# Kernel optimization log

Measured on AMD Instinct MI355X. Metric: run time of the kernel, lower is better.

The kernel has to match this reference:

```python
import jax, jax.numpy as jnp
import numpy as np

B, S, H, I, L, NH = 1, 256, 384, 1536, 2, 8

def _gelu(x):
    return jax.nn.gelu(x, approximate=False)  # torch nn.GELU default = exact erf

def _ln(x, g, b, eps=1e-5):
    m = x.mean(-1, keepdims=True)
    v = jnp.var(x, axis=-1, keepdims=True)
    return (x - m) / jnp.sqrt(v + eps) * g + b

def _mha(x, Wqkv, bqkv, Wo, bo):
    b_, s_, h_ = x.shape
    d = h_ // NH
    qkv = x @ Wqkv.T + bqkv  # [B,S,3H]
    q, k, v = jnp.split(qkv, 3, axis=-1)
    sp = lambda t: t.reshape(b_, s_, NH, d).transpose(0, 2, 1, 3)  # [B,NH,S,d]
    q, k, v = sp(q), sp(k), sp(v)
    att = jax.nn.softmax(jnp.einsum('bhqd,bhkd->bhqk', q * (1.0 / np.sqrt(d)), k), axis=-1)
    o = jnp.einsum('bhqk,bhkd->bhqd', att, v).transpose(0, 2, 1, 3).reshape(b_, s_, h_)
    return o @ Wo.T + bo

def _forward(hidden_states, Wqkv, bqkv, Wo, bo, W1, b1, W2, b2, g1, be1, g2, be2,
             Wbil, bbil, Wc1, bc1, Wc2, bc2, Wih, bih, Whh, bhh, Wp1, bp1, Wp2, bp2,
             Wout, bout, reasoning_steps):
    x = hidden_states
    rstate = jnp.zeros((x.shape[0], x.shape[-1]), x.dtype)
    cprobs, conts = [], []
    for _ in range(reasoning_steps):
        # symbolic reasoning layers (eval mode: dropout off)
        for l in range(L):
            x = _ln(x + _mha(x, Wqkv[l], bqkv[l], Wo[l], bo[l]), g1[l], be1[l])
            ff = _gelu(x @ W1[l].T + b1[l]) @ W2[l].T + b2[l]
            x = _ln(x + ff, g2[l], be2[l])
        # contradiction detector: bilinear over all token pairs
        tmp = jnp.einsum('bix,oxy->bioy', x, Wbil)            # [B,S,H,H]
        inter = jnp.einsum('bioy,bjy->bijo', tmp, x) + bbil   # [B,S,S,H]
        h1 = _gelu(inter @ Wc1.T + bc1)                       # [B,S,S,H]
        logits = jnp.einsum('bijh,h->bij', h1, Wc2[0]) + bc2[0]
        cprobs.append(jax.nn.sigmoid(logits))
        # recursive reasoning controller (GRUCell on mean-pooled states)
        pooled = x.mean(axis=1)
        gi = pooled @ Wih.T + bih
        gh = rstate @ Whh.T + bhh
        ir, iz, inn = jnp.split(gi, 3, axis=-1)
        hr, hz, hn = jnp.split(gh, 3, axis=-1)
        r = jax.nn.sigmoid(ir + hr)
        z = jax.nn.sigmoid(iz + hz)
        n = jnp.tanh(inn + r * hn)
        rstate = (1.0 - z) * n + z * rstate
        conts.append(jax.nn.sigmoid(_gelu(rstate @ Wp1.T + bp1) @ Wp2[0] + bp2[0]))
    final = x @ Wout.T + bout
    return final, jnp.stack(cprobs), jnp.stack(conts)

def setup_inputs():
    key = jax.random.key(0)
    ks = iter(jax.random.split(key, 40))
    rn = lambda shape, s=0.02: jax.random.normal(next(ks), shape, jnp.float32) * s
    return {
        'hidden_states': jax.random.normal(next(ks), (B, S, H), jnp.float32),
        'Wqkv': rn((L, 3 * H, H)), 'bqkv': jnp.zeros((L, 3 * H)),
        'Wo': rn((L, H, H)), 'bo': jnp.zeros((L, H)),
        'W1': rn((L, I, H)), 'b1': jnp.zeros((L, I)),
        'W2': rn((L, H, I)), 'b2': jnp.zeros((L, H)),
        'g1': jnp.ones((L, H)), 'be1': jnp.zeros((L, H)),
        'g2': jnp.ones((L, H)), 'be2': jnp.zeros((L, H)),
        'Wbil': rn((H, H, H)), 'bbil': jnp.zeros((H,)),
        'Wc1': rn((H, H)), 'bc1': jnp.zeros((H,)),
        'Wc2': rn((1, H)), 'bc2': jnp.zeros((1,)),
        'Wih': rn((3 * H, H)), 'bih': jnp.zeros((3 * H,)),
        'Whh': rn((3 * H, H)), 'bhh': jnp.zeros((3 * H,)),
        'Wp1': rn((H, H)), 'bp1': jnp.zeros((H,)),
        'Wp2': rn((1, H)), 'bp2': jnp.zeros((1,)),
        'Wout': rn((H, H)), 'bout': jnp.zeros((H,)),
        'reasoning_steps': 2,
    }

def reference(hidden_states, Wqkv, bqkv, Wo, bo, W1, b1, W2, b2, g1, be1, g2, be2,
              Wbil, bbil, Wc1, bc1, Wc2, bc2, Wih, bih, Whh, bhh, Wp1, bp1, Wp2, bp2,
              Wout, bout, reasoning_steps):
    return _forward(hidden_states, Wqkv, bqkv, Wo, bo, W1, b1, W2, b2, g1, be1, g2, be2,
                    Wbil, bbil, Wc1, bc1, Wc2, bc2, Wih, bih, Whh, bhh, Wp1, bp1, Wp2, bp2,
                    Wout, bout, reasoning_steps)
```

## Files before the change

kernel.cpp:

```cpp
#include <hip/hip_runtime.h>

typedef __attribute__((ext_vector_type(4))) float f32x4;
typedef __attribute__((ext_vector_type(8))) short s16x8;

#define DEVI __device__ __forceinline__

DEVI float b2f(short s) {
  union { float f; unsigned u; } v; v.u = ((unsigned)(unsigned short)s) << 16; return v.f;
}
DEVI short f2b(float f) {
  union { float f; unsigned u; } v; v.f = f;
  unsigned u = v.u;
  u += 0x7FFFu + ((u >> 16) & 1u);
  return (short)(u >> 16);
}
DEVI float gelu_f(float x) {
  float z2 = 1.5957691216f * x * (1.0f + 0.044715f * x * x);
  float e = __expf(z2);
  float th = 1.0f - 2.0f / (e + 1.0f);
  return 0.5f * x * (1.0f + th);
}
DEVI float sigm_f(float x) { return 1.0f / (1.0f + expf(-x)); }

DEVI void gld16(const short* g, const short* l) {
  __builtin_amdgcn_global_load_lds((const __attribute__((address_space(1))) void*)g,
                                   (__attribute__((address_space(3))) void*)l, 16, 0, 0);
}

template<bool BIAS, bool GELU_ACT, bool OUT_BF16>
__global__ __launch_bounds__(256)
void gemm_fast_k(const short* __restrict__ A, const short* __restrict__ B,
                 const float* __restrict__ bias, void* __restrict__ Cv,
                 int M, int N, int K,
                 long long sA, long long sB, long long sC)
{
  __shared__ short As[2][128 * 32];
  __shared__ short Bs[2][128 * 32];
  const int bz = blockIdx.z;
  const int n0 = blockIdx.x * 128;
  const int m0 = blockIdx.y * 128;
  const int t = threadIdx.x, lane = t & 63, wave = t >> 6;
  const int wm = wave >> 1, wn = wave & 1;
  const short* Ab = A + bz * sA;
  const short* Bb = B + bz * sB;
  const int srow = lane >> 2;
  const int scol = (lane & 3) * 8;
  const int fr = lane & 15, fs = lane >> 4;

  f32x4 acc[4][4];
#pragma unroll
  for (int i = 0; i < 4; ++i)
#pragma unroll
    for (int j = 0; j < 4; ++j) acc[i][j] = f32x4{0.f, 0.f, 0.f, 0.f};

  auto stage = [&](int b, int k0) {
#pragma unroll
    for (int q = 0; q < 2; ++q) {
      int c = wave * 2 + q;
      gld16(Ab + (long long)(m0 + c * 16 + srow) * K + k0 + scol, &As[b][c * 512]);
      gld16(Bb + (long long)(n0 + c * 16 + srow) * K + k0 + scol, &Bs[b][c * 512]);
    }
  };

  const int NT = K >> 5;
  stage(0, 0);
  __syncthreads();
  for (int tt = 0; tt < NT; ++tt) {
    const int cur = tt & 1;
    if (tt + 1 < NT) stage(cur ^ 1, (tt + 1) << 5);
    s16x8 af[4], bfv[4];
#pragma unroll
    for (int i = 0; i < 4; ++i) af[i]  = *(const s16x8*)&As[cur][(wm * 64 + i * 16 + fr) * 32 + fs * 8];
#pragma unroll
    for (int j = 0; j < 4; ++j) bfv[j] = *(const s16x8*)&Bs[cur][(wn * 64 + j * 16 + fr) * 32 + fs * 8];
#pragma unroll
    for (int i = 0; i < 4; ++i)
#pragma unroll
      for (int j = 0; j < 4; ++j)
        acc[i][j] = __builtin_amdgcn_mfma_f32_16x16x32_bf16(af[i], bfv[j], acc[i][j], 0, 0, 0);
    if (tt + 1 < NT) __syncthreads();
  }

#pragma unroll
  for (int i = 0; i < 4; ++i) {
    int rowb = m0 + wm * 64 + i * 16 + fs * 4;
#pragma unroll
    for (int j = 0; j < 4; ++j) {
      int col = n0 + wn * 64 + j * 16 + fr;
      float bb = BIAS ? bias[col] : 0.0f;
#pragma unroll
      for (int u = 0; u < 4; ++u) {
        float v = acc[i][j][u] + bb;
        if constexpr (GELU_ACT) v = gelu_f(v);
        long long off = bz * sC + (long long)(rowb + u) * N + col;
        if constexpr (OUT_BF16) ((short*)Cv)[off] = f2b(v);
        else                    ((float*)Cv)[off] = v;
      }
    }
  }
}

template<bool BIAS, bool GELU_ACT, bool OUT_BF16>
__global__ __launch_bounds__(256)
void gemm64_k(const short* __restrict__ A, const short* __restrict__ B,
              const float* __restrict__ bias, void* __restrict__ Cv,
              int M, int N, int K)
{
  __shared__ short As[2][64 * 32];
  __shared__ short Bs[2][64 * 32];
  const int n0 = blockIdx.x * 64;
  const int m0 = blockIdx.y * 64;
  const int t = threadIdx.x, lane = t & 63, wave = t >> 6;
  const int wm = wave >> 1, wn = wave & 1;
  const int srow = lane >> 2;
  const int scol = (lane & 3) * 8;
  const int fr = lane & 15, fs = lane >> 4;

  f32x4 acc[2][2];
#pragma unroll
  for (int i = 0; i < 2; ++i)
#pragma unroll
    for (int j = 0; j < 2; ++j) acc[i][j] = f32x4{0.f, 0.f, 0.f, 0.f};

  auto stage = [&](int b, int k0) {
    gld16(A + (long long)(m0 + wave * 16 + srow) * K + k0 + scol, &As[b][wave * 512]);
    gld16(B + (long long)(n0 + wave * 16 + srow) * K + k0 + scol, &Bs[b][wave * 512]);
  };

  const int NT = K >> 5;
  stage(0, 0);
  __syncthreads();
  for (int tt = 0; tt < NT; ++tt) {
    const int cur = tt & 1;
    if (tt + 1 < NT) stage(cur ^ 1, (tt + 1) << 5);
    s16x8 af[2], bfv[2];
#pragma unroll
    for (int i = 0; i < 2; ++i) af[i]  = *(const s16x8*)&As[cur][(wm * 32 + i * 16 + fr) * 32 + fs * 8];
#pragma unroll
    for (int j = 0; j < 2; ++j) bfv[j] = *(const s16x8*)&Bs[cur][(wn * 32 + j * 16 + fr) * 32 + fs * 8];
#pragma unroll
    for (int i = 0; i < 2; ++i)
#pragma unroll
      for (int j = 0; j < 2; ++j)
        acc[i][j] = __builtin_amdgcn_mfma_f32_16x16x32_bf16(af[i], bfv[j], acc[i][j], 0, 0, 0);
    if (tt + 1 < NT) __syncthreads();
  }

#pragma unroll
  for (int i = 0; i < 2; ++i) {
    int rowb = m0 + wm * 32 + i * 16 + fs * 4;
#pragma unroll
    for (int j = 0; j < 2; ++j) {
      int col = n0 + wn * 32 + j * 16 + fr;
      float bb = BIAS ? bias[col] : 0.0f;
#pragma unroll
      for (int u = 0; u < 4; ++u) {
        float v = acc[i][j][u] + bb;
        if constexpr (GELU_ACT) v = gelu_f(v);
        long long off = (long long)(rowb + u) * N + col;
        if constexpr (OUT_BF16) ((short*)Cv)[off] = f2b(v);
        else                    ((float*)Cv)[off] = v;
      }
    }
  }
}

__global__ __launch_bounds__(256)
void transpose_k(const float* __restrict__ W, short* __restrict__ WT)
{
  __shared__ short L[64 * 68];
  const int o  = blockIdx.z;
  const int x0 = blockIdx.x * 64, y0 = blockIdx.y * 64;
  const float* Wo = W  + (long long)o * 147456;
  short*      WTo = WT + (long long)o * 147456;
  const int t  = threadIdx.x;
  const int rr = t >> 4;
  const int cc = (t & 15) * 4;
#pragma unroll
  for (int q = 0; q < 4; ++q) {
    int xl = rr + 16 * q;
    float4 v = *(const float4*)(Wo + (x0 + xl) * 384 + y0 + cc);
    short4 p; p.x = f2b(v.x); p.y = f2b(v.y); p.z = f2b(v.z); p.w = f2b(v.w);
    *(short4*)&L[xl * 68 + cc] = p;
  }
  __syncthreads();
#pragma unroll
  for (int q = 0; q < 4; ++q) {
    int yl = rr + 16 * q;
    short4 p;
    p.x = L[(cc + 0) * 68 + yl];
    p.y = L[(cc + 1) * 68 + yl];
    p.z = L[(cc + 2) * 68 + yl];
    p.w = L[(cc + 3) * 68 + yl];
    *(short4*)(WTo + (y0 + yl) * 384 + x0 + cc) = p;
  }
}

__global__ __launch_bounds__(256)
void convw_k(const float* __restrict__ W, short* __restrict__ Wb, int n)
{
  int i = (blockIdx.x * 256 + threadIdx.x) * 4;
  if (i < n) {
    float4 v = *(const float4*)(W + i);
    short4 p; p.x = f2b(v.x); p.y = f2b(v.y); p.z = f2b(v.z); p.w = f2b(v.w);
    *(short4*)(Wb + i) = p;
  }
}

__global__ __launch_bounds__(256)
void attn_k(const float* __restrict__ qkv, short* __restrict__ outb)
{
  __shared__ short Ks[256 * 48];
  __shared__ short Vs[256 * 48];
  __shared__ float Ps[32][258];
  const int h  = blockIdx.y;
  const int q0 = blockIdx.x * 32;
  const int t = threadIdx.x, lane = t & 63, wave = t >> 6;
  for (int idx = t; idx < 256 * 48; idx += 256) {
    int j = idx / 48, d = idx - j * 48;
    Ks[idx] = f2b(qkv[j * 1152 + 384 + h * 48 + d]);
    Vs[idx] = f2b(qkv[j * 1152 + 768 + h * 48 + d]);
  }
  __syncthreads();
  const int part = lane & 7;
  const int rl   = wave * 8 + (lane >> 3);
  const int row  = q0 + rl;
  float q[48];
#pragma unroll
  for (int d = 0; d < 48; ++d) q[d] = qkv[row * 1152 + h * 48 + d] * 0.14433756729740644f;
  float mx = -1e30f;
  for (int jj = 0; jj < 32; ++jj) {
    int j = jj * 8 + part;
    float a = 0.f;
#pragma unroll
    for (int dd = 0; dd < 12; ++dd) {
      short4 kk = *(const short4*)&Ks[j * 48 + dd * 4];
      a += q[dd*4+0]*b2f(kk.x) + q[dd*4+1]*b2f(kk.y) + q[dd*4+2]*b2f(kk.z) + q[dd*4+3]*b2f(kk.w);
    }
    Ps[rl][j] = a;
    mx = fmaxf(mx, a);
  }
  mx = fmaxf(mx, __shfl_xor(mx, 1));
  mx = fmaxf(mx, __shfl_xor(mx, 2));
  mx = fmaxf(mx, __shfl_xor(mx, 4));
  float sum = 0.f;
  for (int jj = 0; jj < 32; ++jj) {
    int j = jj * 8 + part;
    float e = expf(Ps[rl][j] - mx);
    Ps[rl][j] = e;
    sum += e;
  }
  sum += __shfl_xor(sum, 1); sum += __shfl_xor(sum, 2); sum += __shfl_xor(sum, 4);
  const float inv = 1.f / sum;
  __syncthreads();
  float o[6] = {0.f, 0.f, 0.f, 0.f, 0.f, 0.f};
  const int vb = part * 6;
  for (int j = 0; j < 256; ++j) {
    float p = Ps[rl][j];
    int base = j * 48 + vb;
#pragma unroll
    for (int dd = 0; dd < 3; ++dd) {
      short2 vv = *(const short2*)&Vs[base + dd * 2];
      o[dd*2]   += p * b2f(vv.x);
      o[dd*2+1] += p * b2f(vv.y);
    }
  }
#pragma unroll
  for (int d = 0; d < 6; ++d) outb[row * 384 + h * 48 + vb + d] = f2b(o[d] * inv);
}

__global__ __launch_bounds__(128)
void ln_k(const float* __restrict__ x, const float* __restrict__ d,
          const float* __restrict__ g, const float* __restrict__ b,
          float* __restrict__ xo, short* __restrict__ xob)
{
  const int row = blockIdx.x, t = threadIdx.x;
  float v[3]; float s = 0.f, ss = 0.f;
#pragma unroll
  for (int i = 0; i < 3; ++i) {
    int c = t + 128 * i;
    float u = x[row * 384 + c] + d[row * 384 + c];
    v[i] = u; s += u; ss += u * u;
  }
#pragma unroll
  for (int m = 1; m < 64; m <<= 1) { s += __shfl_xor(s, m); ss += __shfl_xor(ss, m); }
  __shared__ float sh[4];
  if ((t & 63) == 0) { sh[(t >> 6) * 2] = s; sh[(t >> 6) * 2 + 1] = ss; }
  __syncthreads();
  s = sh[0] + sh[2]; ss = sh[1] + sh[3];
  float mean = s * (1.f / 384.f);
  float var  = ss * (1.f / 384.f) - mean * mean;
  float rstd = rsqrtf(var + 1e-5f);
#pragma unroll
  for (int i = 0; i < 3; ++i) {
    int c = t + 128 * i;
    float y = (v[i] - mean) * rstd * g[c] + b[c];
    xo[row * 384 + c]  = y;
    xob[row * 384 + c] = f2b(y);
  }
}

__global__ void init_k(const float* __restrict__ hs, float* __restrict__ x,
                       short* __restrict__ xb, float* __restrict__ rstate)
{
  int i = blockIdx.x * 256 + threadIdx.x;
  if (i < 98304) { float v = hs[i]; x[i] = v; xb[i] = f2b(v); }
  if (i < 384) rstate[i] = 0.f;
}

__global__ __launch_bounds__(256)
void logits_k(const short* __restrict__ h1, const float* __restrict__ Wc2,
              const float* __restrict__ bc2, float* __restrict__ outp)
{
  const int t = threadIdx.x, lane = t & 63, wave = t >> 6;
  const int row = blockIdx.x * 4 + wave;
  const short* hr = h1 + (long long)row * 384;
  float a = 0.f;
#pragma unroll
  for (int e = 0; e < 6; ++e) { int c = lane + 64 * e; a += b2f(hr[c]) * Wc2[c]; }
#pragma unroll
  for (int m = 1; m < 64; m <<= 1) a += __shfl_xor(a, m);
  if (lane == 0) outp[row] = sigm_f(a + bc2[0]);
}

__global__ __launch_bounds__(384)
void pool1_k(const float* __restrict__ x, float* __restrict__ partial)
{
  const int t = threadIdx.x, p = blockIdx.x;
  float s = 0.f;
  const float* xr = x + p * 32 * 384;
#pragma unroll 4
  for (int i = 0; i < 32; ++i) s += xr[i * 384 + t];
  partial[p * 384 + t] = s;
}

__global__ __launch_bounds__(256)
void gih_k(const float* __restrict__ Wih, const float* __restrict__ bih,
           const float* __restrict__ Whh, const float* __restrict__ bhh,
           const float* __restrict__ partial, const float* __restrict__ rstate,
           float* __restrict__ gi, float* __restrict__ gh)
{
  const int t = threadIdx.x, lane = t & 63, wave = t >> 6;
  const int r = blockIdx.x * 4 + wave;
  float a = 0.f, b = 0.f;
#pragma unroll
  for (int e = 0; e < 6; ++e) {
    int c = lane + 64 * e;
    float pc = 0.f;
#pragma unroll
    for (int p = 0; p < 8; ++p) pc += partial[p * 384 + c];
    pc *= (1.f / 256.f);
    a += Wih[r * 384 + c] * pc;
    b += Whh[r * 384 + c] * rstate[c];
  }
#pragma unroll
  for (int m = 1; m < 64; m <<= 1) { a += __shfl_xor(a, m); b += __shfl_xor(b, m); }
  if (lane == 0) { gi[r] = a + bih[r]; gh[r] = b + bhh[r]; }
}

__global__ __launch_bounds__(384)
void gru2_k(const float* __restrict__ gi, const float* __restrict__ gh,
            float* __restrict__ rstate, float* __restrict__ hnew)
{
  const int t = threadIdx.x;
  float r = sigm_f(gi[t] + gh[t]);
  float z = sigm_f(gi[384 + t] + gh[384 + t]);
  float n = tanhf(gi[768 + t] + r * gh[768 + t]);
  float h = (1.f - z) * n + z * rstate[t];
  rstate[t] = h;
  hnew[t] = h;
}

__global__ __launch_bounds__(256)
void p1_k(const float* __restrict__ Wp1, const float* __restrict__ bp1,
          const float* __restrict__ hnew, float* __restrict__ p1)
{
  const int t = threadIdx.x, lane = t & 63, wave = t >> 6;
  const int r = blockIdx.x * 4 + wave;
  float a = 0.f;
#pragma unroll
  for (int e = 0; e < 6; ++e) { int c = lane + 64 * e; a += Wp1[r * 384 + c] * hnew[c]; }
#pragma unroll
  for (int m = 1; m < 64; m <<= 1) a += __shfl_xor(a, m);
  if (lane == 0) p1[r] = gelu_f(a + bp1[r]);
}

__global__ __launch_bounds__(64)
void cont_k(const float* __restrict__ p1, const float* __restrict__ Wp2,
            const float* __restrict__ bp2, float* __restrict__ out_cont)
{
  const int lane = threadIdx.x;
  float a = 0.f;
#pragma unroll
  for (int e = 0; e < 6; ++e) { int c = lane + 64 * e; a += p1[c] * Wp2[c]; }
#pragma unroll
  for (int m = 1; m < 64; m <<= 1) a += __shfl_xor(a, m);
  if (lane == 0) out_cont[0] = sigm_f(a + bp2[0]);
}

extern "C" void kernel_launch(void* const* d_in, const int* in_sizes, int n_in,
                              void* d_out, int out_size, void* d_ws, size_t ws_size,
                              hipStream_t stream)
{
  const float* hs   = (const float*)d_in[0];
  const float* Wqkv = (const float*)d_in[1];
  const float* bqkv = (const float*)d_in[2];
  const float* Wo   = (const float*)d_in[3];
  const float* bo   = (const float*)d_in[4];
  const float* W1   = (const float*)d_in[5];
  const float* b1   = (const float*)d_in[6];
  const float* W2   = (const float*)d_in[7];
  const float* b2   = (const float*)d_in[8];
  const float* g1   = (const float*)d_in[9];
  const float* be1  = (const float*)d_in[10];
  const float* g2   = (const float*)d_in[11];
  const float* be2  = (const float*)d_in[12];
  const float* Wbil = (const float*)d_in[13];
  const float* bbil = (const float*)d_in[14];
  const float* Wc1  = (const float*)d_in[15];
  const float* bc1  = (const float*)d_in[16];
  const float* Wc2  = (const float*)d_in[17];
  const float* bc2  = (const float*)d_in[18];
  const float* Wih  = (const float*)d_in[19];
  const float* bih  = (const float*)d_in[20];
  const float* Whh  = (const float*)d_in[21];
  const float* bhh  = (const float*)d_in[22];
  const float* Wp1  = (const float*)d_in[23];
  const float* bp1  = (const float*)d_in[24];
  const float* Wp2  = (const float*)d_in[25];
  const float* bp2  = (const float*)d_in[26];
  const float* Wout = (const float*)d_in[27];
  const float* bout = (const float*)d_in[28];
  float* out = (float*)d_out;

  char* ws = (char*)d_ws;
  size_t off = 0;
  auto alloc = [&](size_t bytes) -> char* {
    char* p = ws + off; off += (bytes + 255) & ~(size_t)255; return p;
  };
  short* wbilT   = (short*)alloc(56623104ULL * 2);
  short* tmp     = (short*)alloc(256ULL * 147456 * 2);
  short* inter   = (short*)alloc(256ULL * 98304 * 2);
  float* x       = (float*)alloc(98304 * 4);
  short* xb      = (short*)alloc(98304 * 2);
  float* qkv     = (float*)alloc(294912 * 4);
  short* attnb   = (short*)alloc(98304 * 2);
  float* delta   = (float*)alloc(98304 * 4);
  short* ff1b    = (short*)alloc(393216 * 2);
  float* rstate  = (float*)alloc(384 * 4);
  float* partial = (float*)alloc(8 * 384 * 4);
  float* gi      = (float*)alloc(1152 * 4);
  float* gh      = (float*)alloc(1152 * 4);
  float* hnew    = (float*)alloc(384 * 4);
  float* p1buf   = (float*)alloc(384 * 4);
  short* wc1b    = (short*)alloc(147456 * 2);
  short* wqkvb   = (short*)alloc(884736ULL * 2);
  short* wob     = (short*)alloc(294912ULL * 2);
  short* w1b     = (short*)alloc(1179648ULL * 2);
  short* w2b     = (short*)alloc(1179648ULL * 2);
  short* woutb   = (short*)alloc(147456 * 2);
  short* h1 = tmp;
  (void)ws_size; (void)in_sizes; (void)n_in; (void)out_size;

  dim3 B256(256);

  init_k<<<dim3(384), B256, 0, stream>>>(hs, x, xb, rstate);
  transpose_k<<<dim3(6, 6, 384), B256, 0, stream>>>(Wbil, wbilT);
  convw_k<<<dim3(144),  B256, 0, stream>>>(Wc1, wc1b, 147456);
  convw_k<<<dim3(864),  B256, 0, stream>>>(Wqkv, wqkvb, 884736);
  convw_k<<<dim3(288),  B256, 0, stream>>>(Wo, wob, 294912);
  convw_k<<<dim3(1152), B256, 0, stream>>>(W1, w1b, 1179648);
  convw_k<<<dim3(1152), B256, 0, stream>>>(W2, w2b, 1179648);
  convw_k<<<dim3(144),  B256, 0, stream>>>(Wout, woutb, 147456);

  for (int s = 0; s < 2; ++s) {
    for (int l = 0; l < 2; ++l) {
      gemm64_k<true, false, false><<<dim3(18, 4), B256, 0, stream>>>(
          xb, wqkvb + l * 442368, bqkv + l * 1152, qkv, 256, 1152, 384);
      attn_k<<<dim3(8, 8), B256, 0, stream>>>(qkv, attnb);
      gemm64_k<true, false, false><<<dim3(6, 4), B256, 0, stream>>>(
          attnb, wob + l * 147456, bo + l * 384, delta, 256, 384, 384);
      ln_k<<<dim3(256), dim3(128), 0, stream>>>(x, delta, g1 + l * 384, be1 + l * 384, x, xb);
      gemm64_k<true, true, true><<<dim3(24, 4), B256, 0, stream>>>(
          xb, w1b + l * 589824, b1 + l * 1536, ff1b, 256, 1536, 384);
      gemm64_k<true, false, false><<<dim3(6, 4), B256, 0, stream>>>(
          ff1b, w2b + l * 589824, b2 + l * 384, delta, 256, 384, 1536);
      ln_k<<<dim3(256), dim3(128), 0, stream>>>(x, delta, g2 + l * 384, be2 + l * 384, x, xb);
    }
    gemm_fast_k<false, false, true><<<dim3(1152, 2, 1), B256, 0, stream>>>(
        xb, wbilT, (const float*)nullptr, tmp, 256, 147456, 384, 0, 0, 0);
    gemm_fast_k<true, false, true><<<dim3(3, 2, 256), B256, 0, stream>>>(
        xb, tmp, bbil, inter, 256, 384, 384, 0, 147456LL, 98304LL);
    gemm_fast_k<true, true, true><<<dim3(3, 2, 256), B256, 0, stream>>>(
        inter, wc1b, bc1, h1, 256, 384, 384, 98304LL, 0, 98304LL);
    logits_k<<<dim3(16384), B256, 0, stream>>>(h1, Wc2, bc2, out + 98304 + s * 65536);
    pool1_k<<<dim3(8), dim3(384), 0, stream>>>(x, partial);
    gih_k<<<dim3(288), B256, 0, stream>>>(Wih, bih, Whh, bhh, partial, rstate, gi, gh);
    gru2_k<<<dim3(1), dim3(384), 0, stream>>>(gi, gh, rstate, hnew);
    p1_k<<<dim3(96), B256, 0, stream>>>(Wp1, bp1, hnew, p1buf);
    cont_k<<<dim3(1), dim3(64), 0, stream>>>(p1buf, Wp2, bp2, out + 98304 + 131072 + s);
  }
  gemm64_k<true, false, false><<<dim3(6, 4), B256, 0, stream>>>(
      xb, woutb, bout, out, 256, 384, 384);
}
```

Measured before the change: 693.7 us.

## Use 256-row GEMM tiles and fuse Wc1 GEMM with GELU and logits reduction

```diff
diff --git a/kernel.cpp b/kernel.cpp
--- a/kernel.cpp
+++ b/kernel.cpp
@@ -27,24 +27,23 @@
                                    (__attribute__((address_space(3))) void*)l, 16, 0, 0);
 }
 
-template<bool BIAS, bool GELU_ACT, bool OUT_BF16>
-__global__ __launch_bounds__(256)
-void gemm_fast_k(const short* __restrict__ A, const short* __restrict__ B,
-                 const float* __restrict__ bias, void* __restrict__ Cv,
-                 int M, int N, int K,
-                 long long sA, long long sB, long long sC)
-{
-  __shared__ short As[2][128 * 32];
+template<bool BIAS, bool OUT_BF16>
+__global__ __launch_bounds__(512)
+void gemm256_k(const short* __restrict__ A, const short* __restrict__ B,
+               const float* __restrict__ bias, void* __restrict__ Cv,
+               int N, int K,
+               long long sA, long long sB, long long sC)
+{
+  __shared__ short As[2][256 * 32];
   __shared__ short Bs[2][128 * 32];
   const int bz = blockIdx.z;
   const int n0 = blockIdx.x * 128;
-  const int m0 = blockIdx.y * 128;
   const int t = threadIdx.x, lane = t & 63, wave = t >> 6;
   const int wm = wave >> 1, wn = wave & 1;
   const short* Ab = A + bz * sA;
   const short* Bb = B + bz * sB;
-  const int srow = lane >> 2;
-  const int scol = (lane & 3) * 8;
+  const int lr = lane >> 2;
+  const int lc = (lane & 3) * 8;
   const int fr = lane & 15, fs = lane >> 4;
 
   f32x4 acc[4][4];
@@ -55,11 +54,11 @@
 
   auto stage = [&](int b, int k0) {
 #pragma unroll
-    for (int q = 0; q < 2; ++q) {
-      int c = wave * 2 + q;
-      gld16(Ab + (long long)(m0 + c * 16 + srow) * K + k0 + scol, &As[b][c * 512]);
-      gld16(Bb + (long long)(n0 + c * 16 + srow) * K + k0 + scol, &Bs[b][c * 512]);
-    }
+    for (int q = 0; q < 2; ++q)
+      gld16(Ab + (long long)(q * 128 + wave * 16 + lr) * K + k0 + lc,
+            &As[b][(q * 128 + wave * 16) * 32]);
+    gld16(Bb + (long long)(n0 + wave * 16 + lr) * K + k0 + lc,
+          &Bs[b][wave * 16 * 32]);
   };
 
   const int NT = K >> 5;
@@ -83,7 +82,7 @@
 
 #pragma unroll
   for (int i = 0; i < 4; ++i) {
-    int rowb = m0 + wm * 64 + i * 16 + fs * 4;
+    int rowb = wm * 64 + i * 16 + fs * 4;
 #pragma unroll
     for (int j = 0; j < 4; ++j) {
       int col = n0 + wn * 64 + j * 16 + fr;
@@ -91,13 +90,90 @@
 #pragma unroll
       for (int u = 0; u < 4; ++u) {
         float v = acc[i][j][u] + bb;
-        if constexpr (GELU_ACT) v = gelu_f(v);
         long long off = bz * sC + (long long)(rowb + u) * N + col;
         if constexpr (OUT_BF16) ((short*)Cv)[off] = f2b(v);
         else                    ((float*)Cv)[off] = v;
       }
     }
   }
+}
+
+__global__ __launch_bounds__(512)
+void h1log256_k(const short* __restrict__ inter, const short* __restrict__ Wc1b,
+                const float* __restrict__ bc1, const float* __restrict__ Wc2,
+                const float* __restrict__ bc2, float* __restrict__ outp)
+{
+  __shared__ short As[2][256 * 32];
+  __shared__ short Bs[2][128 * 32];
+  __shared__ float part[256][2];
+  const int ib = blockIdx.x;
+  const int t = threadIdx.x, lane = t & 63, wave = t >> 6;
+  const int wm = wave >> 1, wn = wave & 1;
+  const short* Ab = inter + (long long)ib * 98304;
+  const int lr = lane >> 2;
+  const int lc = (lane & 3) * 8;
+  const int fr = lane & 15, fs = lane >> 4;
+
+  float lp[16];
+#pragma unroll
+  for (int e = 0; e < 16; ++e) lp[e] = 0.f;
+
+  for (int n0 = 0; n0 < 384; n0 += 128) {
+    f32x4 acc[4][4];
+#pragma unroll
+    for (int i = 0; i < 4; ++i)
+#pragma unroll
+      for (int j = 0; j < 4; ++j) acc[i][j] = f32x4{0.f, 0.f, 0.f, 0.f};
+
+    auto stage = [&](int b, int k0) {
+#pragma unroll
+      for (int q = 0; q < 2; ++q)
+        gld16(Ab + (long long)(q * 128 + wave * 16 + lr) * 384 + k0 + lc,
+              &As[b][(q * 128 + wave * 16) * 32]);
+      gld16(Wc1b + (long long)(n0 + wave * 16 + lr) * 384 + k0 + lc,
+            &Bs[b][wave * 16 * 32]);
+    };
+
+    stage(0, 0);
+    __syncthreads();
+    for (int tt = 0; tt < 12; ++tt) {
+      const int cur = tt & 1;
+      if (tt + 1 < 12) stage(cur ^ 1, (tt + 1) << 5);
+      s16x8 af[4], bfv[4];
+#pragma unroll
+      for (int i = 0; i < 4; ++i) af[i]  = *(const s16x8*)&As[cur][(wm * 64 + i * 16 + fr) * 32 + fs * 8];
+#pragma unroll
+      for (int j = 0; j < 4; ++j) bfv[j] = *(const s16x8*)&Bs[cur][(wn * 64 + j * 16 + fr) * 32 + fs * 8];
+#pragma unroll
+      for (int i = 0; i < 4; ++i)
+#pragma unroll
+        for (int j = 0; j < 4; ++j)
+          acc[i][j] = __builtin_amdgcn_mfma_f32_16x16x32_bf16(af[i], bfv[j], acc[i][j], 0, 0, 0);
+      if (tt + 1 < 12) __syncthreads();
+    }
+#pragma unroll
+    for (int i = 0; i < 4; ++i)
+#pragma unroll
+      for (int j = 0; j < 4; ++j) {
+        int col = n0 + wn * 64 + j * 16 + fr;
+        float w2 = Wc2[col], b1v = bc1[col];
+#pragma unroll
+        for (int u = 0; u < 4; ++u)
+          lp[i * 4 + u] += gelu_f(acc[i][j][u] + b1v) * w2;
+      }
+    __syncthreads();
+  }
+#pragma unroll
+  for (int m = 1; m < 16; m <<= 1)
+#pragma unroll
+    for (int e = 0; e < 16; ++e) lp[e] += __shfl_xor(lp[e], m);
+  if (fr == 0) {
+#pragma unroll
+    for (int e = 0; e < 16; ++e)
+      part[wm * 64 + (e >> 2) * 16 + fs * 4 + (e & 3)][wn] = lp[e];
+  }
+  __syncthreads();
+  if (t < 256) outp[ib * 256 + t] = sigm_f(part[t][0] + part[t][1] + bc2[0]);
 }
 
 template<bool BIAS, bool GELU_ACT, bool OUT_BF16>
@@ -306,21 +382,6 @@
   int i = blockIdx.x * 256 + threadIdx.x;
   if (i < 98304) { float v = hs[i]; x[i] = v; xb[i] = f2b(v); }
   if (i < 384) rstate[i] = 0.f;
-}
-
-__global__ __launch_bounds__(256)
-void logits_k(const short* __restrict__ h1, const float* __restrict__ Wc2,
-              const float* __restrict__ bc2, float* __restrict__ outp)
-{
-  const int t = threadIdx.x, lane = t & 63, wave = t >> 6;
-  const int row = blockIdx.x * 4 + wave;
-  const short* hr = h1 + (long long)row * 384;
-  float a = 0.f;
-#pragma unroll
-  for (int e = 0; e < 6; ++e) { int c = lane + 64 * e; a += b2f(hr[c]) * Wc2[c]; }
-#pragma unroll
-  for (int m = 1; m < 64; m <<= 1) a += __shfl_xor(a, m);
-  if (lane == 0) outp[row] = sigm_f(a + bc2[0]);
 }
 
 __global__ __launch_bounds__(384)
@@ -459,10 +520,10 @@
   short* w1b     = (short*)alloc(1179648ULL * 2);
   short* w2b     = (short*)alloc(1179648ULL * 2);
   short* woutb   = (short*)alloc(147456 * 2);
-  short* h1 = tmp;
   (void)ws_size; (void)in_sizes; (void)n_in; (void)out_size;
 
   dim3 B256(256);
+  dim3 B512(512);
 
   init_k<<<dim3(384), B256, 0, stream>>>(hs, x, xb, rstate);
   transpose_k<<<dim3(6, 6, 384), B256, 0, stream>>>(Wbil, wbilT);
@@ -487,13 +548,12 @@
           ff1b, w2b + l * 589824, b2 + l * 384, delta, 256, 384, 1536);
       ln_k<<<dim3(256), dim3(128), 0, stream>>>(x, delta, g2 + l * 384, be2 + l * 384, x, xb);
     }
-    gemm_fast_k<false, false, true><<<dim3(1152, 2, 1), B256, 0, stream>>>(
-        xb, wbilT, (const float*)nullptr, tmp, 256, 147456, 384, 0, 0, 0);
-    gemm_fast_k<true, false, true><<<dim3(3, 2, 256), B256, 0, stream>>>(
-        xb, tmp, bbil, inter, 256, 384, 384, 0, 147456LL, 98304LL);
-    gemm_fast_k<true, true, true><<<dim3(3, 2, 256), B256, 0, stream>>>(
-        inter, wc1b, bc1, h1, 256, 384, 384, 98304LL, 0, 98304LL);
-    logits_k<<<dim3(16384), B256, 0, stream>>>(h1, Wc2, bc2, out + 98304 + s * 65536);
+    gemm256_k<false, true><<<dim3(1152, 1, 1), B512, 0, stream>>>(
+        xb, wbilT, (const float*)nullptr, tmp, 147456, 384, 0, 0, 0);
+    gemm256_k<true, true><<<dim3(3, 1, 256), B512, 0, stream>>>(
+        xb, tmp, bbil, inter, 384, 384, 0, 147456LL, 98304LL);
+    h1log256_k<<<dim3(256), B512, 0, stream>>>(inter, wc1b, bc1, Wc2, bc2,
+                                               out + 98304 + s * 65536);
     pool1_k<<<dim3(8), dim3(384), 0, stream>>>(x, partial);
     gih_k<<<dim3(288), B256, 0, stream>>>(Wih, bih, Whh, bhh, partial, rstate, gi, gh);
     gru2_k<<<dim3(1), dim3(384), 0, stream>>>(gi, gh, rstate, hnew);
```

After: 671.9 us. 3.1% less time.
